# Performance work log

Hardware: AMD Instinct MI355X
Metric: run time of the kernel (lower is better)

## Reference

```python
import jax, jax.numpy as jnp
import numpy as np

N0, N1, N2 = 200000, 100000, 50000
E0, E1 = 1600000, 800000
IN_F, H_F, N_CLS = 128, 256, 64


def sage_conv(h_src, src_idx, dst_idx, num_dst, W_self, W_neigh, b):
    # DGL SAGEConv with aggregator_type='mean':
    #   h_neigh = mean over in-neighbors of h_src
    #   out = h_dst @ W_self + h_neigh @ W_neigh + b
    h_dst = h_src[:num_dst]
    msgs = h_src[src_idx]                                   # [E, F] gather
    summed = jax.ops.segment_sum(msgs, dst_idx, num_segments=num_dst)
    deg = jax.ops.segment_sum(jnp.ones((src_idx.shape[0],), h_src.dtype),
                              dst_idx, num_segments=num_dst)
    h_neigh = summed / jnp.maximum(deg, 1.0)[:, None]       # mean, safe for deg=0
    return h_dst @ W_self + h_neigh @ W_neigh + b


def setup_inputs() -> dict:
    key = jax.random.key(0)
    ks = jax.random.split(key, 10)
    s1 = 1.0 / np.sqrt(IN_F)
    s2 = 1.0 / np.sqrt(H_F)
    return {
        "x": jax.random.normal(ks[0], (N0, IN_F), jnp.float32),
        "src0": jax.random.randint(ks[1], (E0,), 0, N0, jnp.int64 if jax.config.jax_enable_x64 else jnp.int32),
        "dst0": jnp.sort(jax.random.randint(ks[2], (E0,), 0, N1)),
        "src1": jax.random.randint(ks[3], (E1,), 0, N1),
        "dst1": jnp.sort(jax.random.randint(ks[4], (E1,), 0, N2)),
        "num_dst0": N1,
        "num_dst1": N2,
        "W_self1": jax.random.normal(ks[5], (IN_F, H_F), jnp.float32) * s1,
        "W_neigh1": jax.random.normal(ks[6], (IN_F, H_F), jnp.float32) * s1,
        "b1": jnp.zeros((H_F,), jnp.float32),
        "W_self2": jax.random.normal(ks[7], (H_F, N_CLS), jnp.float32) * s2,
        "W_neigh2": jax.random.normal(ks[8], (H_F, N_CLS), jnp.float32) * s2,
        "b2": jnp.zeros((N_CLS,), jnp.float32),
    }


def reference(x, src0, dst0, src1, dst1, num_dst0, num_dst1,
              W_self1, W_neigh1, b1, W_self2, W_neigh2, b2):
    h = sage_conv(x, src0, dst0, num_dst0, W_self1, W_neigh1, b1)   # [N1, H]
    h = jax.nn.relu(h)
    h = sage_conv(h, src1, dst1, num_dst1, W_self2, W_neigh2, b2)   # [N2, C]
    return h
```

## Files before the change

### kernel.cpp

```cpp
#include <hip/hip_runtime.h>

constexpr int cN1  = 100000;
constexpr int cN2  = 50000;
constexpr int cE0  = 1600000;
constexpr int cE1  = 800000;
constexpr int cIN  = 128;
constexpr int cH   = 256;
constexpr int cCLS = 64;

using bf16x8 = __attribute__((ext_vector_type(8))) short;
using f32x4  = __attribute__((ext_vector_type(4))) float;

__device__ __forceinline__ float bflo(unsigned int u) {
    union { unsigned int i; float f; } v; v.i = u << 16; return v.f;
}
__device__ __forceinline__ float bfhi(unsigned int u) {
    union { unsigned int i; float f; } v; v.i = u & 0xFFFF0000u; return v.f;
}
__device__ __forceinline__ unsigned int f2bf(float f) {
    union { float f; unsigned int i; } v; v.f = f;
    return (v.i + 0x7FFFu + ((v.i >> 16) & 1u)) >> 16;
}

__global__ void build_rows(const int* __restrict__ dst, int E, int num_dst,
                           int* __restrict__ row_start) {
    int d = blockIdx.x * blockDim.x + threadIdx.x;
    if (d > num_dst) return;
    int lo = 0, hi = E;
    while (lo < hi) {
        int mid = (lo + hi) >> 1;
        if (dst[mid] < d) lo = mid + 1; else hi = mid;
    }
    row_start[d] = lo;
}

__global__ __launch_bounds__(256) void cvt_bf16(const float* __restrict__ in,
                                                unsigned short* __restrict__ out,
                                                int n8) {
    int i = blockIdx.x * 256 + threadIdx.x;
    if (i >= n8) return;
    const float4* p = (const float4*)in + (size_t)i * 2;
    float4 a = p[0], b = p[1];
    uint4 o;
    o.x = f2bf(a.x) | (f2bf(a.y) << 16);
    o.y = f2bf(a.z) | (f2bf(a.w) << 16);
    o.z = f2bf(b.x) | (f2bf(b.y) << 16);
    o.w = f2bf(b.z) | (f2bf(b.w) << 16);
    ((uint4*)out)[i] = o;
}

__global__ void cvt_w(const float* __restrict__ Ws1, const float* __restrict__ Wn1,
                      const float* __restrict__ Wn2, const float* __restrict__ Ws2,
                      unsigned short* __restrict__ Wt1,
                      unsigned short* __restrict__ Wt2n,
                      unsigned short* __restrict__ Wt2s) {
    int i = blockIdx.x * 256 + threadIdx.x;
    if (i < 256 * 256) {
        int n = i / 256, k = i % 256;
        float v = (k < 128) ? Ws1[k * 256 + n] : Wn1[(k - 128) * 256 + n];
        Wt1[n * 256 + k] = (unsigned short)f2bf(v);
    } else if (i < 256 * 256 + 64 * 256) {
        int j = i - 65536; int n = j / 256, k = j % 256;
        Wt2n[n * 256 + k] = (unsigned short)f2bf(Wn2[k * 64 + n]);
    } else if (i < 256 * 256 + 2 * 64 * 256) {
        int j = i - 65536 - 16384; int n = j / 256, k = j % 256;
        Wt2s[n * 256 + k] = (unsigned short)f2bf(Ws2[k * 64 + n]);
    }
}

template<int K, bool ACCUM>
__global__ __launch_bounds__(256) void agg_bf16(
        const unsigned short* __restrict__ src,
        const int* __restrict__ sidx,
        const int* __restrict__ rows,
        void* __restrict__ outv, int num_dst) {
    constexpr int LPR = K / 8;
    constexpr int RPB = 256 / LPR;
    constexpr int R4  = K / 8;
    const int tid = threadIdx.x;
    const int g = tid / LPR, t = tid % LPR;
    const int m = blockIdx.x * RPB + g;
    if (m >= num_dst) return;

    const uint4* s4 = (const uint4*)src;
    const int e0 = rows[m], e1 = rows[m + 1];
    float acc[8];
    #pragma unroll
    for (int j = 0; j < 8; ++j) acc[j] = 0.f;

    auto addv = [&](uint4 v) {
        acc[0] += bflo(v.x); acc[1] += bfhi(v.x);
        acc[2] += bflo(v.y); acc[3] += bfhi(v.y);
        acc[4] += bflo(v.z); acc[5] += bfhi(v.z);
        acc[6] += bflo(v.w); acc[7] += bfhi(v.w);
    };

    int e = e0;
    for (; e + 4 <= e1; e += 4) {
        int s0 = sidx[e], s1 = sidx[e + 1], s2 = sidx[e + 2], s3 = sidx[e + 3];
        uint4 v0 = s4[(size_t)s0 * R4 + t];
        uint4 v1 = s4[(size_t)s1 * R4 + t];
        uint4 v2 = s4[(size_t)s2 * R4 + t];
        uint4 v3 = s4[(size_t)s3 * R4 + t];
        addv(v0); addv(v1); addv(v2); addv(v3);
    }
    for (; e < e1; ++e) addv(s4[(size_t)sidx[e] * R4 + t]);

    const int deg = e1 - e0;
    const float inv = 1.0f / (float)(deg > 1 ? deg : 1);
    if (!ACCUM) {
        uint4 o;
        o.x = f2bf(acc[0] * inv) | (f2bf(acc[1] * inv) << 16);
        o.y = f2bf(acc[2] * inv) | (f2bf(acc[3] * inv) << 16);
        o.z = f2bf(acc[4] * inv) | (f2bf(acc[5] * inv) << 16);
        o.w = f2bf(acc[6] * inv) | (f2bf(acc[7] * inv) << 16);
        ((uint4*)outv)[(size_t)m * R4 + t] = o;
    } else {
        float* op = (float*)outv + (size_t)m * K + t * 8;
        float4 o0 = *(float4*)op, o1 = *(float4*)(op + 4);
        o0.x += acc[0] * inv; o0.y += acc[1] * inv;
        o0.z += acc[2] * inv; o0.w += acc[3] * inv;
        o1.x += acc[4] * inv; o1.y += acc[5] * inv;
        o1.z += acc[6] * inv; o1.w += acc[7] * inv;
        *(float4*)op = o0; *(float4*)(op + 4) = o1;
    }
}

template<int BM, int BN, int WM, int WN, bool RELU, bool HASBIAS, bool OUTBF16>
__global__ __launch_bounds__(256) void gemm_mfma(
        const unsigned short* __restrict__ A1, int K1,
        const unsigned short* __restrict__ A2, int K2,
        const unsigned short* __restrict__ Bt,
        const float* __restrict__ bias,
        void* __restrict__ Cout, int M, int N) {
    static_assert(2 * WM * 16 == BM && 2 * WN * 16 == BN, "wave tiling");
    __shared__ unsigned short As[BM][40];
    __shared__ unsigned short Bs[BN][40];

    const int tid = threadIdx.x;
    const int m0 = blockIdx.x * BM, n0 = blockIdx.y * BN;
    const int lane = tid & 63, wave = tid >> 6;
    const int wrow = wave >> 1, wcol = wave & 1;
    const int quad = lane >> 4, l16 = lane & 15;
    const int K = K1 + K2;

    f32x4 acc[WM][WN];
    #pragma unroll
    for (int i = 0; i < WM; ++i)
        #pragma unroll
        for (int j = 0; j < WN; ++j)
            acc[i][j] = (f32x4){0.f, 0.f, 0.f, 0.f};

    for (int kb = 0; kb < K; kb += 32) {
        const unsigned short* Ab; int lda, kloc;
        if (kb < K1) { Ab = A1; lda = K1; kloc = kb; }
        else         { Ab = A2; lda = K2; kloc = kb - K1; }

        #pragma unroll
        for (int f = 0; f < (BM * 4) / 256; ++f) {
            int idx = tid + f * 256;
            int row = idx >> 2, q = idx & 3;
            int gm = m0 + row;
            uint4 v = make_uint4(0, 0, 0, 0);
            if (gm < M) v = *(const uint4*)(Ab + (size_t)gm * lda + kloc + q * 8);
            *(uint4*)&As[row][q * 8] = v;
        }
        #pragma unroll
        for (int f = 0; f < (BN * 4) / 256; ++f) {
            int idx = tid + f * 256;
            int row = idx >> 2, q = idx & 3;
            uint4 v = *(const uint4*)(Bt + (size_t)(n0 + row) * K + kb + q * 8);
            *(uint4*)&Bs[row][q * 8] = v;
        }
        __syncthreads();

        bf16x8 a[WM], b[WN];
        #pragma unroll
        for (int i = 0; i < WM; ++i)
            a[i] = *(const bf16x8*)&As[(wrow * WM + i) * 16 + l16][quad * 8];
        #pragma unroll
        for (int j = 0; j < WN; ++j)
            b[j] = *(const bf16x8*)&Bs[(wcol * WN + j) * 16 + l16][quad * 8];
        #pragma unroll
        for (int i = 0; i < WM; ++i)
            #pragma unroll
            for (int j = 0; j < WN; ++j)
                acc[i][j] = __builtin_amdgcn_mfma_f32_16x16x32_bf16(
                    a[i], b[j], acc[i][j], 0, 0, 0);
        __syncthreads();
    }

    float bv[WN];
    #pragma unroll
    for (int j = 0; j < WN; ++j)
        bv[j] = HASBIAS ? bias[n0 + (wcol * WN + j) * 16 + l16] : 0.f;
    #pragma unroll
    for (int i = 0; i < WM; ++i) {
        #pragma unroll
        for (int r = 0; r < 4; ++r) {
            int gm = m0 + (wrow * WM + i) * 16 + quad * 4 + r;
            if (gm >= M) continue;
            #pragma unroll
            for (int j = 0; j < WN; ++j) {
                int gn = n0 + (wcol * WN + j) * 16 + l16;
                float v = acc[i][j][r] + bv[j];
                if (RELU) v = fmaxf(v, 0.f);
                if (OUTBF16)
                    ((unsigned short*)Cout)[(size_t)gm * N + gn] = (unsigned short)f2bf(v);
                else
                    ((float*)Cout)[(size_t)gm * N + gn] = v;
            }
        }
    }
}

extern "C" void kernel_launch(void* const* d_in, const int* in_sizes, int n_in,
                              void* d_out, int out_size, void* d_ws, size_t ws_size,
                              hipStream_t stream) {
    const float* x      = (const float*)d_in[0];
    const int*   src0   = (const int*)d_in[1];
    const int*   dst0   = (const int*)d_in[2];
    const int*   src1   = (const int*)d_in[3];
    const int*   dst1   = (const int*)d_in[4];
    const float* Wself1  = (const float*)d_in[7];
    const float* Wneigh1 = (const float*)d_in[8];
    const float* b1      = (const float*)d_in[9];
    const float* Wself2  = (const float*)d_in[10];
    const float* Wneigh2 = (const float*)d_in[11];
    const float* b2      = (const float*)d_in[12];
    float* out = (float*)d_out;

    char* ws = (char*)d_ws;
    int* row0 = (int*)ws;
    int* row1 = row0 + (cN1 + 1);
    size_t off = (size_t)((cN1 + 1) + (cN2 + 1)) * sizeof(int);
    off = (off + 1023) & ~(size_t)1023;
    unsigned short* xb  = (unsigned short*)(ws + off);  off += (size_t)200000 * cIN * 2;
    unsigned short* nb  = (unsigned short*)(ws + off);  off += (size_t)cN1 * cIN * 2;
    unsigned short* h1b = (unsigned short*)(ws + off);  off += (size_t)cN1 * cH * 2;
    unsigned short* zb  = (unsigned short*)(ws + off);  off += (size_t)cN1 * cCLS * 2;
    unsigned short* Wt1  = (unsigned short*)(ws + off); off += 256 * 256 * 2;
    unsigned short* Wt2n = (unsigned short*)(ws + off); off += 64 * 256 * 2;
    unsigned short* Wt2s = (unsigned short*)(ws + off); off += 64 * 256 * 2;

    build_rows<<<(cN1 + 1 + 255) / 256, 256, 0, stream>>>(dst0, cE0, cN1, row0);
    build_rows<<<(cN2 + 1 + 255) / 256, 256, 0, stream>>>(dst1, cE1, cN2, row1);

    cvt_bf16<<<(200000 * cIN / 8 + 255) / 256, 256, 0, stream>>>(x, xb, 200000 * cIN / 8);
    cvt_w<<<(256 * 256 + 2 * 64 * 256 + 255) / 256, 256, 0, stream>>>(
        Wself1, Wneigh1, Wneigh2, Wself2, Wt1, Wt2n, Wt2s);

    agg_bf16<cIN, false><<<(cN1 + 15) / 16, 256, 0, stream>>>(
        xb, src0, row0, nb, cN1);
    gemm_mfma<128, 128, 4, 4, true, true, true>
        <<<dim3((cN1 + 127) / 128, cH / 128), 256, 0, stream>>>(
        xb, cIN, nb, cIN, Wt1, b1, h1b, cN1, cH);

    gemm_mfma<128, 64, 4, 2, false, false, true>
        <<<dim3((cN1 + 127) / 128, 1), 256, 0, stream>>>(
        h1b, cH, nullptr, 0, Wt2n, nullptr, zb, cN1, cCLS);
    gemm_mfma<128, 64, 4, 2, false, true, false>
        <<<dim3((cN2 + 127) / 128, 1), 256, 0, stream>>>(
        h1b, cH, nullptr, 0, Wt2s, b2, out, cN2, cCLS);
    agg_bf16<cCLS, true><<<(cN2 + 31) / 32, 256, 0, stream>>>(
        zb, src1, row1, out, cN2);
}
```

Before: 347.2 us.

## Aggregate neighbors with one wavefront per destination row, splitting edges across lanes

The mean-aggregation kernel now gives each destination row a full 64-lane wavefront. Sub-groups of lanes each handle different edges in parallel, and the partial sums are combined with xor-shuffle reductions. Before, a small lane group walked each row's edges serially. The aim is more memory-level parallelism in the gather, since each row has only about 16 neighbors on average. In exchange it adds shuffle reduction work, launches more blocks, and leaves many lanes idle when the final write happens or a row has few edges.

```diff
diff --git a/kernel.cpp b/kernel.cpp
--- a/kernel.cpp
+++ b/kernel.cpp
@@ -69,21 +69,23 @@
 }
 
 template<int K, bool ACCUM>
-__global__ __launch_bounds__(256) void agg_bf16(
+__global__ __launch_bounds__(256) void agg_wave(
         const unsigned short* __restrict__ src,
         const int* __restrict__ sidx,
         const int* __restrict__ rows,
         void* __restrict__ outv, int num_dst) {
     constexpr int LPR = K / 8;
-    constexpr int RPB = 256 / LPR;
-    constexpr int R4  = K / 8;
+    constexpr int EPW = 64 / LPR;
     const int tid = threadIdx.x;
-    const int g = tid / LPR, t = tid % LPR;
-    const int m = blockIdx.x * RPB + g;
+    const int lane = tid & 63;
+    const int m = blockIdx.x * 4 + (tid >> 6);
     if (m >= num_dst) return;
+    const int sub = lane / LPR;
+    const int t   = lane % LPR;
 
     const uint4* s4 = (const uint4*)src;
     const int e0 = rows[m], e1 = rows[m + 1];
+
     float acc[8];
     #pragma unroll
     for (int j = 0; j < 8; ++j) acc[j] = 0.f;
@@ -95,34 +97,48 @@
         acc[6] += bflo(v.w); acc[7] += bfhi(v.w);
     };
 
-    int e = e0;
-    for (; e + 4 <= e1; e += 4) {
-        int s0 = sidx[e], s1 = sidx[e + 1], s2 = sidx[e + 2], s3 = sidx[e + 3];
-        uint4 v0 = s4[(size_t)s0 * R4 + t];
-        uint4 v1 = s4[(size_t)s1 * R4 + t];
-        uint4 v2 = s4[(size_t)s2 * R4 + t];
-        uint4 v3 = s4[(size_t)s3 * R4 + t];
-        addv(v0); addv(v1); addv(v2); addv(v3);
-    }
-    for (; e < e1; ++e) addv(s4[(size_t)sidx[e] * R4 + t]);
-
-    const int deg = e1 - e0;
-    const float inv = 1.0f / (float)(deg > 1 ? deg : 1);
-    if (!ACCUM) {
-        uint4 o;
-        o.x = f2bf(acc[0] * inv) | (f2bf(acc[1] * inv) << 16);
-        o.y = f2bf(acc[2] * inv) | (f2bf(acc[3] * inv) << 16);
-        o.z = f2bf(acc[4] * inv) | (f2bf(acc[5] * inv) << 16);
-        o.w = f2bf(acc[6] * inv) | (f2bf(acc[7] * inv) << 16);
-        ((uint4*)outv)[(size_t)m * R4 + t] = o;
-    } else {
-        float* op = (float*)outv + (size_t)m * K + t * 8;
-        float4 o0 = *(float4*)op, o1 = *(float4*)(op + 4);
-        o0.x += acc[0] * inv; o0.y += acc[1] * inv;
-        o0.z += acc[2] * inv; o0.w += acc[3] * inv;
-        o1.x += acc[4] * inv; o1.y += acc[5] * inv;
-        o1.z += acc[6] * inv; o1.w += acc[7] * inv;
-        *(float4*)op = o0; *(float4*)(op + 4) = o1;
+    int base = e0;
+    for (; base + 2 * EPW <= e1; base += 2 * EPW) {
+        const int sA = sidx[base + sub];
+        const int sB = sidx[base + EPW + sub];
+        uint4 vA = s4[(size_t)sA * LPR + t];
+        uint4 vB = s4[(size_t)sB * LPR + t];
+        addv(vA); addv(vB);
+    }
+    for (; base < e1; base += EPW) {
+        const int idx = base + sub;
+        if (idx < e1) {
+            const int s = sidx[idx];
+            addv(s4[(size_t)s * LPR + t]);
+        }
+    }
+
+    #pragma unroll
+    for (int j = 0; j < 8; ++j) {
+        #pragma unroll
+        for (int off = LPR; off < 64; off <<= 1)
+            acc[j] += __shfl_xor(acc[j], off, 64);
+    }
+
+    if (sub == 0) {
+        const int deg = e1 - e0;
+        const float inv = 1.0f / (float)(deg > 1 ? deg : 1);
+        if (!ACCUM) {
+            uint4 o;
+            o.x = f2bf(acc[0] * inv) | (f2bf(acc[1] * inv) << 16);
+            o.y = f2bf(acc[2] * inv) | (f2bf(acc[3] * inv) << 16);
+            o.z = f2bf(acc[4] * inv) | (f2bf(acc[5] * inv) << 16);
+            o.w = f2bf(acc[6] * inv) | (f2bf(acc[7] * inv) << 16);
+            ((uint4*)outv)[(size_t)m * LPR + t] = o;
+        } else {
+            float* op = (float*)outv + (size_t)m * K + t * 8;
+            float4 o0 = *(float4*)op, o1 = *(float4*)(op + 4);
+            o0.x += acc[0] * inv; o0.y += acc[1] * inv;
+            o0.z += acc[2] * inv; o0.w += acc[3] * inv;
+            o1.x += acc[4] * inv; o1.y += acc[5] * inv;
+            o1.z += acc[6] * inv; o1.w += acc[7] * inv;
+            *(float4*)op = o0; *(float4*)(op + 4) = o1;
+        }
     }
 }
 
@@ -250,7 +266,7 @@
     cvt_w<<<(256 * 256 + 2 * 64 * 256 + 255) / 256, 256, 0, stream>>>(
         Wself1, Wneigh1, Wneigh2, Wself2, Wt1, Wt2n, Wt2s);
 
-    agg_bf16<cIN, false><<<(cN1 + 15) / 16, 256, 0, stream>>>(
+    agg_wave<cIN, false><<<(cN1 + 3) / 4, 256, 0, stream>>>(
         xb, src0, row0, nb, cN1);
     gemm_mfma<128, 128, 4, 4, true, true, true>
         <<<dim3((cN1 + 127) / 128, cH / 128), 256, 0, stream>>>(
@@ -262,6 +278,6 @@
     gemm_mfma<128, 64, 4, 2, false, true, false>
         <<<dim3((cN2 + 127) / 128, 1), 256, 0, stream>>>(
         h1b, cH, nullptr, 0, Wt2s, b2, out, cN2, cCLS);
-    agg_bf16<cCLS, true><<<(cN2 + 31) / 32, 256, 0, stream>>>(
+    agg_wave<cCLS, true><<<(cN2 + 3) / 4, 256, 0, stream>>>(
         zb, src1, row1, out, cN2);
 }
```

Result: slower. 356.8 us (+2.7%).
